# Kernel tuning notes

Hardware: AMD Instinct MI355X
Metric: run time of the kernel (lower is better)

## Reference

```python
import jax, jax.numpy as jnp
import numpy as np

def binarize(t):
    # deterministic sign binarization to {-1, +1}
    return jnp.where(t >= 0, 1.0, -1.0).astype(t.dtype)

def setup_inputs() -> dict:
    key = jax.random.key(0)
    k1, k2 = jax.random.split(key)
    x = jax.random.normal(k1, (8192, 4096), dtype=jnp.float32)
    kernel = jax.random.normal(k2, (4096, 4096), dtype=jnp.float32)
    return {"x": x, "kernel": kernel}

def reference(x, kernel):
    # BinaryLayer.call with binary=True: matmul(binarize(x), binarize(W))
    return jnp.matmul(binarize(x), binarize(kernel))
```

## Files before the change

kernel.cpp:

```cpp
#include <hip/hip_runtime.h>
#include <stdint.h>

#define MDIM 8192
#define NDIM 4096
#define KDIM 4096
#define KB2  (KDIM / 2)
#define BKB  128
#define NKT  (KDIM / 256)

#define BM 256
#define BN 256
#define ABUF      32768
#define BUFSTRIDE 65536

typedef __attribute__((ext_vector_type(4)))  int   i32x4;
typedef __attribute__((ext_vector_type(8)))  int   i32x8;
typedef __attribute__((ext_vector_type(16))) float f32x16;

__device__ __forceinline__ void gload16(const void* g, void* l) {
    __builtin_amdgcn_global_load_lds(
        (const __attribute__((address_space(1))) void*)g,
        (__attribute__((address_space(3))) void*)l, 16, 0, 0);
}

__device__ __forceinline__ i32x8 pad8(i32x4 v) {
    i32x8 r;
    r[0] = v[0]; r[1] = v[1]; r[2] = v[2]; r[3] = v[3];
    r[4] = 0;    r[5] = 0;    r[6] = 0;    r[7] = 0;
    return r;
}

#define MFMA_FP4_32(a, b, c)                                                 \
    __builtin_amdgcn_mfma_scale_f32_32x32x64_f8f6f4(                          \
        (a), (b), (c), 4, 4, 0, 0x7F7F7F7F, 0, 0x7F7F7F7F)

__global__ __launch_bounds__(256) void pack_a4_kernel(const float* __restrict__ X,
                                                      uint8_t* __restrict__ A4) {
    size_t gt = (size_t)blockIdx.x * 256 + threadIdx.x;
    const float4* x4 = (const float4*)X + gt * 4;
    uint32_t out[2] = {0, 0};
#pragma unroll
    for (int q = 0; q < 4; ++q) {
        float4 v = x4[q];
        uint32_t b0 = (v.x >= 0.f ? 0x2u : 0xAu) | ((v.y >= 0.f ? 0x2u : 0xAu) << 4);
        uint32_t b1 = (v.z >= 0.f ? 0x2u : 0xAu) | ((v.w >= 0.f ? 0x2u : 0xAu) << 4);
        out[q >> 1] |= (b0 | (b1 << 8)) << ((q & 1) * 16);
    }
    ((uint2*)A4)[gt] = make_uint2(out[0], out[1]);
}

__global__ __launch_bounds__(256) void pack_b4t_kernel(const float* __restrict__ W,
                                                       uint8_t* __restrict__ B4) {
    __shared__ uint8_t t[64][72];
    const int tid = threadIdx.x;
    const int k0 = blockIdx.y * 64, n0 = blockIdx.x * 64;
#pragma unroll
    for (int r = 0; r < 4; ++r) {
        int e  = r * 1024 + tid * 4;
        int k  = e >> 6;
        int nn = e & 63;
        float4 v = *(const float4*)&W[(size_t)(k0 + k) * NDIM + n0 + nn];
        uint32_t b0 = (v.x >= 0.f) ? 0x2u : 0xAu;
        uint32_t b1 = (v.y >= 0.f) ? 0x2u : 0xAu;
        uint32_t b2 = (v.z >= 0.f) ? 0x2u : 0xAu;
        uint32_t b3 = (v.w >= 0.f) ? 0x2u : 0xAu;
        *(uint32_t*)&t[k][nn] = b0 | (b1 << 8) | (b2 << 16) | (b3 << 24);
    }
    __syncthreads();
    const int n = tid >> 2, kc = tid & 3;
    uint32_t w[2] = {0, 0};
#pragma unroll
    for (int b = 0; b < 8; ++b) {
        int k = kc * 16 + b * 2;
        uint32_t byte = (uint32_t)t[k][n] | ((uint32_t)t[k + 1][n] << 4);
        w[b >> 2] |= byte << ((b & 3) * 8);
    }
    *(uint2*)&B4[(size_t)(n0 + n) * KB2 + k0 / 2 + kc * 8] = make_uint2(w[0], w[1]);
}

__global__ __launch_bounds__(512, 2) void binmm_fp4_kernel(const uint8_t* __restrict__ A4,
                                                           const uint8_t* __restrict__ B4,
                                                           float* __restrict__ C) {
    __shared__ uint8_t lds[2 * BUFSTRIDE];

    const int tid = threadIdx.x, lane = tid & 63, wid = tid >> 6;
    const int wr = wid >> 2, wc = wid & 3;
    const int l31 = lane & 31, kh = lane >> 5;
    const int m0 = blockIdx.y * BM, n0 = blockIdx.x * BN;

    const int srow  = tid >> 3;
    const int sslot = tid & 7;
    const uint8_t* gA[4];
    const uint8_t* gB[4];
#pragma unroll
    for (int p = 0; p < 4; ++p) {
        int row = srow + p * 64;
        int ss  = (sslot ^ (row & 7)) * 16;
        gA[p] = A4 + (size_t)(m0 + row) * KB2 + ss;
        gB[p] = B4 + (size_t)(n0 + row) * KB2 + ss;
    }

    f32x16 acc[4][2];
#pragma unroll
    for (int m = 0; m < 4; ++m)
#pragma unroll
        for (int n = 0; n < 2; ++n)
#pragma unroll
            for (int e = 0; e < 16; ++e) acc[m][n][e] = 0.f;

    auto stageA = [&](int nxt) {
#pragma unroll
        for (int p = 0; p < 4; ++p) {
            gload16(gA[p], lds + nxt + tid * 16 + p * 8192);
            gA[p] += BKB;
        }
    };
    auto stageB = [&](int nxt) {
#pragma unroll
        for (int p = 0; p < 4; ++p) {
            gload16(gB[p], lds + nxt + ABUF + tid * 16 + p * 8192);
            gB[p] += BKB;
        }
    };

#define RDA(dst, cur, s) do {                                                  \
        _Pragma("unroll")                                                      \
        for (int mf = 0; mf < 4; ++mf) {                                       \
            int row = wr * 128 + mf * 32 + l31;                                \
            dst[mf] = *(const i32x4*)(lds + (cur) + row * 128 +                \
                                      ((((s) * 2 + kh) ^ (row & 7)) * 16));    \
        }                                                                      \
    } while (0)
#define RDB(dst, cur, s) do {                                                  \
        _Pragma("unroll")                                                      \
        for (int nf = 0; nf < 2; ++nf) {                                       \
            int row = wc * 64 + nf * 32 + l31;                                 \
            dst[nf] = *(const i32x4*)(lds + (cur) + ABUF + row * 128 +         \
                                      ((((s) * 2 + kh) ^ (row & 7)) * 16));    \
        }                                                                      \
    } while (0)
#define CLUSTER(AS, BS) do {                                                   \
        __builtin_amdgcn_s_setprio(1);                                         \
        _Pragma("unroll")                                                      \
        for (int mf = 0; mf < 4; ++mf) {                                       \
            i32x8 a8 = pad8(AS[mf]);                                           \
            acc[mf][0] = MFMA_FP4_32(a8, pad8(BS[0]), acc[mf][0]);             \
            acc[mf][1] = MFMA_FP4_32(a8, pad8(BS[1]), acc[mf][1]);             \
        }                                                                      \
        __builtin_amdgcn_s_setprio(0);                                         \
    } while (0)

    auto tile = [&](int cur, int nxt, bool do_stage) {
        i32x4 aP[4], bP[2], aQ[4], bQ[2];
        RDA(aP, cur, 0); RDB(bP, cur, 0);
        if (do_stage) stageA(nxt);
        RDA(aQ, cur, 1); RDB(bQ, cur, 1);
        CLUSTER(aP, bP);
        if (do_stage) stageB(nxt);
        RDA(aP, cur, 2); RDB(bP, cur, 2);
        CLUSTER(aQ, bQ);
        RDA(aQ, cur, 3); RDB(bQ, cur, 3);
        CLUSTER(aP, bP);
        CLUSTER(aQ, bQ);
        __syncthreads();
    };

    stageA(0); stageB(0);
    __syncthreads();

#pragma unroll 1
    for (int tt = 0; tt < NKT / 2 - 1; ++tt) {
        tile(0, BUFSTRIDE, true);
        tile(BUFSTRIDE, 0, true);
    }
    tile(0, BUFSTRIDE, true);
    tile(BUFSTRIDE, 0, false);

#pragma unroll
    for (int mf = 0; mf < 4; ++mf) {
#pragma unroll
        for (int nf = 0; nf < 2; ++nf) {
            size_t cc = (size_t)(n0 + wc * 64 + nf * 32 + l31);
            int rbase = m0 + wr * 128 + mf * 32 + 4 * kh;
#pragma unroll
            for (int reg = 0; reg < 16; ++reg) {
                int rr = (reg & 3) + 8 * (reg >> 2);
                C[(size_t)(rbase + rr) * NDIM + cc] = acc[mf][nf][reg];
            }
        }
    }
}

extern "C" void kernel_launch(void* const* d_in, const int* in_sizes, int n_in,
                              void* d_out, int out_size, void* d_ws, size_t ws_size,
                              hipStream_t stream) {
    const float* x = (const float*)d_in[0];
    const float* w = (const float*)d_in[1];
    float* out = (float*)d_out;

    uint8_t* A4 = (uint8_t*)d_ws;
    uint8_t* B4 = (uint8_t*)d_ws + (size_t)MDIM * KB2;

    pack_a4_kernel<<<(int)((size_t)MDIM * KDIM / 16 / 256), 256, 0, stream>>>(x, A4);
    pack_b4t_kernel<<<dim3(NDIM / 64, KDIM / 64), 256, 0, stream>>>(w, B4);
    binmm_fp4_kernel<<<dim3(NDIM / BN, MDIM / BM), 512, 0, stream>>>(A4, B4, out);
}
```

Baseline: 122.8 us.

## Switch FP4 GEMM to 16x16x128 MFMA with cross-tile register prefetch

```diff
diff --git a/kernel.cpp b/kernel.cpp
--- a/kernel.cpp
+++ b/kernel.cpp
@@ -13,9 +13,9 @@
 #define ABUF      32768
 #define BUFSTRIDE 65536
 
-typedef __attribute__((ext_vector_type(4)))  int   i32x4;
-typedef __attribute__((ext_vector_type(8)))  int   i32x8;
-typedef __attribute__((ext_vector_type(16))) float f32x16;
+typedef __attribute__((ext_vector_type(4))) int   i32x4;
+typedef __attribute__((ext_vector_type(8))) int   i32x8;
+typedef __attribute__((ext_vector_type(4))) float f32x4;
 
 __device__ __forceinline__ void gload16(const void* g, void* l) {
     __builtin_amdgcn_global_load_lds(
@@ -30,8 +30,8 @@
     return r;
 }
 
-#define MFMA_FP4_32(a, b, c)                                                 \
-    __builtin_amdgcn_mfma_scale_f32_32x32x64_f8f6f4(                          \
+#define MFMA_FP4(a, b, c)                                                   \
+    __builtin_amdgcn_mfma_scale_f32_16x16x128_f8f6f4(                        \
         (a), (b), (c), 4, 4, 0, 0x7F7F7F7F, 0, 0x7F7F7F7F)
 
 __global__ __launch_bounds__(256) void pack_a4_kernel(const float* __restrict__ X,
@@ -85,7 +85,7 @@
 
     const int tid = threadIdx.x, lane = tid & 63, wid = tid >> 6;
     const int wr = wid >> 2, wc = wid & 3;
-    const int l31 = lane & 31, kh = lane >> 5;
+    const int l15 = lane & 15, g = (lane >> 4) & 3;
     const int m0 = blockIdx.y * BM, n0 = blockIdx.x * BN;
 
     const int srow  = tid >> 3;
@@ -100,13 +100,11 @@
         gB[p] = B4 + (size_t)(n0 + row) * KB2 + ss;
     }
 
-    f32x16 acc[4][2];
-#pragma unroll
-    for (int m = 0; m < 4; ++m)
-#pragma unroll
-        for (int n = 0; n < 2; ++n)
-#pragma unroll
-            for (int e = 0; e < 16; ++e) acc[m][n][e] = 0.f;
+    f32x4 acc[8][4];
+#pragma unroll
+    for (int m = 0; m < 8; ++m)
+#pragma unroll
+        for (int n = 0; n < 4; ++n) acc[m][n] = (f32x4){0.f, 0.f, 0.f, 0.f};
 
     auto stageA = [&](int nxt) {
 #pragma unroll
@@ -123,70 +121,79 @@
         }
     };
 
-#define RDA(dst, cur, s) do {                                                  \
+#define RD_A(dst, buf, s, half) do {                                           \
         _Pragma("unroll")                                                      \
         for (int mf = 0; mf < 4; ++mf) {                                       \
-            int row = wr * 128 + mf * 32 + l31;                                \
-            dst[mf] = *(const i32x4*)(lds + (cur) + row * 128 +                \
-                                      ((((s) * 2 + kh) ^ (row & 7)) * 16));    \
+            int row = wr * 128 + (half) * 64 + mf * 16 + l15;                  \
+            dst[mf] = *(const i32x4*)(lds + (buf) + row * 128 +                \
+                                      ((((s) * 4 + g) ^ (row & 7)) * 16));     \
         }                                                                      \
     } while (0)
-#define RDB(dst, cur, s) do {                                                  \
+#define RD_B(dst, buf, s) do {                                                 \
         _Pragma("unroll")                                                      \
-        for (int nf = 0; nf < 2; ++nf) {                                       \
-            int row = wc * 64 + nf * 32 + l31;                                 \
-            dst[nf] = *(const i32x4*)(lds + (cur) + ABUF + row * 128 +         \
-                                      ((((s) * 2 + kh) ^ (row & 7)) * 16));    \
+        for (int nf = 0; nf < 4; ++nf) {                                       \
+            int row = wc * 64 + nf * 16 + l15;                                 \
+            dst[nf] = *(const i32x4*)(lds + (buf) + ABUF + row * 128 +         \
+                                      ((((s) * 4 + g) ^ (row & 7)) * 16));     \
         }                                                                      \
     } while (0)
-#define CLUSTER(AS, BS) do {                                                   \
+#define CLUSTER(AS, BS, half) do {                                             \
         __builtin_amdgcn_s_setprio(1);                                         \
         _Pragma("unroll")                                                      \
         for (int mf = 0; mf < 4; ++mf) {                                       \
             i32x8 a8 = pad8(AS[mf]);                                           \
-            acc[mf][0] = MFMA_FP4_32(a8, pad8(BS[0]), acc[mf][0]);             \
-            acc[mf][1] = MFMA_FP4_32(a8, pad8(BS[1]), acc[mf][1]);             \
+            acc[(half) * 4 + mf][0] = MFMA_FP4(a8, pad8(BS[0]), acc[(half) * 4 + mf][0]); \
+            acc[(half) * 4 + mf][1] = MFMA_FP4(a8, pad8(BS[1]), acc[(half) * 4 + mf][1]); \
+            acc[(half) * 4 + mf][2] = MFMA_FP4(a8, pad8(BS[2]), acc[(half) * 4 + mf][2]); \
+            acc[(half) * 4 + mf][3] = MFMA_FP4(a8, pad8(BS[3]), acc[(half) * 4 + mf][3]); \
         }                                                                      \
         __builtin_amdgcn_s_setprio(0);                                         \
     } while (0)
 
-    auto tile = [&](int cur, int nxt, bool do_stage) {
-        i32x4 aP[4], bP[2], aQ[4], bQ[2];
-        RDA(aP, cur, 0); RDB(bP, cur, 0);
+    i32x4 aLo[4], aHi[4], bC[4];
+    i32x4 aLoN[4], aHiN[4], bN[4];
+
+    auto tile = [&](int cur, int nxt, bool do_stage, bool rd_next) {
+        RD_B(bN, cur, 1);
+        RD_A(aLoN, cur, 1, 0);
         if (do_stage) stageA(nxt);
-        RDA(aQ, cur, 1); RDB(bQ, cur, 1);
-        CLUSTER(aP, bP);
+        CLUSTER(aLo, bC, 0);
+        RD_A(aHiN, cur, 1, 1);
         if (do_stage) stageB(nxt);
-        RDA(aP, cur, 2); RDB(bP, cur, 2);
-        CLUSTER(aQ, bQ);
-        RDA(aQ, cur, 3); RDB(bQ, cur, 3);
-        CLUSTER(aP, bP);
-        CLUSTER(aQ, bQ);
+        CLUSTER(aHi, bC, 1);
+        CLUSTER(aLoN, bN, 0);
+        CLUSTER(aHiN, bN, 1);
         __syncthreads();
+        if (rd_next) {
+            RD_B(bC, nxt, 0);
+            RD_A(aLo, nxt, 0, 0);
+            RD_A(aHi, nxt, 0, 1);
+        }
     };
 
     stageA(0); stageB(0);
     __syncthreads();
+    RD_B(bC, 0, 0);
+    RD_A(aLo, 0, 0, 0);
+    RD_A(aHi, 0, 0, 1);
 
 #pragma unroll 1
     for (int tt = 0; tt < NKT / 2 - 1; ++tt) {
-        tile(0, BUFSTRIDE, true);
-        tile(BUFSTRIDE, 0, true);
-    }
-    tile(0, BUFSTRIDE, true);
-    tile(BUFSTRIDE, 0, false);
-
-#pragma unroll
-    for (int mf = 0; mf < 4; ++mf) {
-#pragma unroll
-        for (int nf = 0; nf < 2; ++nf) {
-            size_t cc = (size_t)(n0 + wc * 64 + nf * 32 + l31);
-            int rbase = m0 + wr * 128 + mf * 32 + 4 * kh;
-#pragma unroll
-            for (int reg = 0; reg < 16; ++reg) {
-                int rr = (reg & 3) + 8 * (reg >> 2);
-                C[(size_t)(rbase + rr) * NDIM + cc] = acc[mf][nf][reg];
-            }
+        tile(0, BUFSTRIDE, true, true);
+        tile(BUFSTRIDE, 0, true, true);
+    }
+    tile(0, BUFSTRIDE, true, true);
+    tile(BUFSTRIDE, 0, false, false);
+
+#pragma unroll
+    for (int mf = 0; mf < 8; ++mf) {
+#pragma unroll
+        for (int nf = 0; nf < 4; ++nf) {
+            size_t cc = (size_t)(n0 + wc * 64 + nf * 16 + l15);
+            int rbase = m0 + wr * 128 + mf * 16 + g * 4;
+#pragma unroll
+            for (int reg = 0; reg < 4; ++reg)
+                C[(size_t)(rbase + reg) * NDIM + cc] = acc[mf][nf][reg];
         }
     }
 }
```

Measured after the change: 145.3 us. 1.18x slower.
